# Performance work log

Hardware: AMD Instinct MI355X
Metric: run time of the kernel (lower is better)

The kernel has to match this reference:

```python
import jax, jax.numpy as jnp
import numpy as np

GRID_SIZE = 5
GRID_LO, GRID_HI = -1.0, 1.0


def setup_inputs() -> dict:
    key = jax.random.key(0)
    k1, k2 = jax.random.split(key)
    B, out_dim, in_dim, H, W = 8, 64, 64, 192, 192
    G = GRID_SIZE + 1
    x = jax.random.normal(k1, (B, in_dim, H, W), dtype=jnp.float32)
    coef = jax.random.normal(k2, (B, out_dim, in_dim, G), dtype=jnp.float32) * 0.1
    return {"x": x, "coef": coef}


def reference(x, coef):
    # x: [B, in_dim, H, W]; coef: [B, out_dim, in_dim, G] with G = grid_size + 1
    G = GRID_SIZE + 1
    grid = jnp.linspace(GRID_LO, GRID_HI, G, dtype=x.dtype)
    lo, hi = grid[0], grid[-1]
    spacing = grid[1] - grid[0]

    B, in_dim, H, W = x.shape
    out_dim = coef.shape[1]
    P = H * W

    xf = x.reshape(B, in_dim, P)
    xc = jnp.clip(xf, lo, hi)
    nx = (xc - lo) / spacing                      # normalized coordinate in [0, grid_size]
    idx = jnp.clip(jnp.floor(nx).astype(jnp.int32), 0, GRID_SIZE - 1)  # left knot
    frac = nx - idx.astype(x.dtype)               # fractional offset (grad flows via nx)
    w1 = 1.0 - frac
    w2 = frac
    idx_next = jnp.clip(idx + 1, 0, GRID_SIZE)    # right knot (max index = G-1)

    # Two-hot interpolation weights over the G grid points: [B, in, P, G]
    Wt = (w1[..., None] * jax.nn.one_hot(idx, G, dtype=x.dtype)
          + w2[..., None] * jax.nn.one_hot(idx_next, G, dtype=x.dtype))

    # result[b,o,p] = sum_i sum_g Wt[b,i,p,g] * coef[b,o,i,g]
    out = jnp.einsum('bipg,boig->bop', Wt, coef)
    return out.reshape(B, out_dim, H, W)
```

## Files before the change

kernel.cpp:

```cpp
#include <hip/hip_runtime.h>
#include <stdint.h>


typedef __fp16 half8_t __attribute__((ext_vector_type(8)));
typedef __fp16 half2_t __attribute__((ext_vector_type(2)));
typedef float f32x4 __attribute__((ext_vector_type(4)));

#define NBATCH 8
#define OD 64
#define ID 64
#define PIX 36864
#define NG 6
#define PT 192
#define KI 16
#define NCHUNK 4
#define AROW 104
#define XROW 18
#define PTILES (PIX / PT)

__global__ __launch_bounds__(256, 2)
void kan_mfma(const float* __restrict__ x, const float* __restrict__ coef,
              float* __restrict__ out) {
  const int t = threadIdx.x;
  const int lane = t & 63;
  const int wave = t >> 6;
  const int q8 = lane >> 4;
  const int col = lane & 15;

  const int bid = blockIdx.x;
  const int b = bid / PTILES;
  const int ptile = bid % PTILES;
  const int p0 = ptile * PT;

  __shared__ __fp16 A_lds[OD][AROW] __attribute__((aligned(16)));
  __shared__ float nx_lds[PT][XROW] __attribute__((aligned(16)));

  f32x4 acc[4][3];
#pragma unroll
  for (int i = 0; i < 4; ++i)
#pragma unroll
    for (int j = 0; j < 3; ++j)
      acc[i][j] = (f32x4){0.f, 0.f, 0.f, 0.f};

  const float* xb = x + (size_t)b * ID * PIX + p0;
  const float* cb = coef + (size_t)b * OD * ID * NG;

  const int iof0 = (q8 & 1) * 8;
  const int ghalf = q8 >> 1;

  for (int c = 0; c < NCHUNK; ++c) {
    const int i0 = c * KI;
    __syncthreads();

#pragma unroll
    for (int j = 0; j < (KI * PT) / 256; ++j) {
      int lin = j * 256 + t;
      int p = lin % PT;
      int iof = lin / PT;
      float xv = xb[(size_t)(i0 + iof) * PIX + p];
      xv = fminf(fmaxf(xv, -1.f), 1.f);
      nx_lds[p][iof] = (xv + 1.f) * 2.5f;
    }

    {
      const int o = t >> 2;
      const int r0 = (t & 3) * 24;
      const float* crow = cb + o * (ID * NG) + i0 * NG + r0;
#pragma unroll
      for (int j = 0; j < 24; ++j) {
        int r = r0 + j;
        int iof = r / 6;
        int g = r - iof * 6;
        A_lds[o][g * KI + iof] = (__fp16)crow[j];
      }
    }
    __syncthreads();

    float nxv[3][8];
#pragma unroll
    for (int pti = 0; pti < 3; ++pti) {
      int p = wave * 48 + pti * 16 + col;
#pragma unroll
      for (int j = 0; j < 8; ++j)
        nxv[pti][j] = nx_lds[p][iof0 + j];
    }

#pragma unroll
    for (int ks = 0; ks < 3; ++ks) {
      half8_t af[4];
#pragma unroll
      for (int ot = 0; ot < 4; ++ot)
        af[ot] = *(const half8_t*)&A_lds[ot * 16 + col][ks * 32 + q8 * 8];

      const float gf = (float)(2 * ks + ghalf);
#pragma unroll
      for (int pti = 0; pti < 3; ++pti) {
        union { half2_t h2[4]; half8_t v; } bu;
#pragma unroll
        for (int jj = 0; jj < 4; ++jj) {
          float h0 = fmaxf(0.f, 1.f - fabsf(nxv[pti][2 * jj] - gf));
          float h1 = fmaxf(0.f, 1.f - fabsf(nxv[pti][2 * jj + 1] - gf));
          bu.h2[jj] = __builtin_amdgcn_cvt_pkrtz(h0, h1);
        }
#pragma unroll
        for (int ot = 0; ot < 4; ++ot)
          acc[ot][pti] = __builtin_amdgcn_mfma_f32_16x16x32_f16(
              af[ot], bu.v, acc[ot][pti], 0, 0, 0);
      }
    }
  }

  float* ob = out + (size_t)b * OD * PIX + p0;
#pragma unroll
  for (int ot = 0; ot < 4; ++ot) {
#pragma unroll
    for (int pti = 0; pti < 3; ++pti) {
      int p = wave * 48 + pti * 16 + col;
#pragma unroll
      for (int r = 0; r < 4; ++r) {
        int o = ot * 16 + q8 * 4 + r;
        ob[(size_t)o * PIX + p] = acc[ot][pti][r];
      }
    }
  }
}

extern "C" void kernel_launch(void* const* d_in, const int* in_sizes, int n_in,
                              void* d_out, int out_size, void* d_ws, size_t ws_size,
                              hipStream_t stream) {
  const float* x = (const float*)d_in[0];
  const float* coef = (const float*)d_in[1];
  float* out = (float*)d_out;
  dim3 grid(NBATCH * PTILES);
  dim3 block(256);
  hipLaunchKernelGGL(kan_mfma, grid, block, 0, stream, x, coef, out);
}
```

Measured before the change: 154.0 us.

## Stage all coef once in LDS and load x directly into registers

The full per-batch coefficient block for all four input chunks is now loaded once into a wider LDS array with vectorized float4 loads and packed half2 stores, replacing the per-chunk scalar staging. The x tile is no longer staged through LDS: each lane reads its own pixels straight from global memory. This removes the per-chunk barriers. Occupancy hint is raised to 3 blocks per SM and output stores are made nontemporal. Direct x loads are strided per lane, so coalescing depends on the 16-lane col pattern, and the larger LDS footprint may limit occupancy.

```diff
diff --git a/kernel.cpp b/kernel.cpp
--- a/kernel.cpp
+++ b/kernel.cpp
@@ -14,11 +14,11 @@
 #define PT 192
 #define KI 16
 #define NCHUNK 4
-#define AROW 104
-#define XROW 18
+#define KC (KI * NG)
+#define AROW 392
 #define PTILES (PIX / PT)
 
-__global__ __launch_bounds__(256, 2)
+__global__ __launch_bounds__(256, 3)
 void kan_mfma(const float* __restrict__ x, const float* __restrict__ coef,
               float* __restrict__ out) {
   const int t = threadIdx.x;
@@ -33,7 +33,26 @@
   const int p0 = ptile * PT;
 
   __shared__ __fp16 A_lds[OD][AROW] __attribute__((aligned(16)));
-  __shared__ float nx_lds[PT][XROW] __attribute__((aligned(16)));
+
+  {
+    const int o = t >> 2;
+    const int c = t & 3;
+    const float* crow = coef + (size_t)b * (OD * ID * NG) + o * (ID * NG) + c * KC;
+    __fp16* arow = &A_lds[o][c * KC];
+#pragma unroll
+    for (int blk = 0; blk < 8; ++blk) {
+      f32x4 va = ((const f32x4*)crow)[blk * 3 + 0];
+      f32x4 vb = ((const f32x4*)crow)[blk * 3 + 1];
+      f32x4 vc = ((const f32x4*)crow)[blk * 3 + 2];
+      const float lo[NG] = {va[0], va[1], va[2], va[3], vb[0], vb[1]};
+      const float hi[NG] = {vb[2], vb[3], vc[0], vc[1], vc[2], vc[3]};
+#pragma unroll
+      for (int g = 0; g < NG; ++g) {
+        half2_t h2 = __builtin_amdgcn_cvt_pkrtz(lo[g], hi[g]);
+        *(half2_t*)&arow[g * KI + blk * 2] = h2;
+      }
+    }
+  }
 
   f32x4 acc[4][3];
 #pragma unroll
@@ -42,47 +61,26 @@
     for (int j = 0; j < 3; ++j)
       acc[i][j] = (f32x4){0.f, 0.f, 0.f, 0.f};
 
-  const float* xb = x + (size_t)b * ID * PIX + p0;
-  const float* cb = coef + (size_t)b * OD * ID * NG;
+  __syncthreads();
 
   const int iof0 = (q8 & 1) * 8;
   const int ghalf = q8 >> 1;
-
-  for (int c = 0; c < NCHUNK; ++c) {
-    const int i0 = c * KI;
-    __syncthreads();
+  const float* xb = x + (size_t)b * ID * PIX + p0 + wave * 48 + col
+                      + (size_t)iof0 * PIX;
 
 #pragma unroll
-    for (int j = 0; j < (KI * PT) / 256; ++j) {
-      int lin = j * 256 + t;
-      int p = lin % PT;
-      int iof = lin / PT;
-      float xv = xb[(size_t)(i0 + iof) * PIX + p];
-      xv = fminf(fmaxf(xv, -1.f), 1.f);
-      nx_lds[p][iof] = (xv + 1.f) * 2.5f;
-    }
-
-    {
-      const int o = t >> 2;
-      const int r0 = (t & 3) * 24;
-      const float* crow = cb + o * (ID * NG) + i0 * NG + r0;
-#pragma unroll
-      for (int j = 0; j < 24; ++j) {
-        int r = r0 + j;
-        int iof = r / 6;
-        int g = r - iof * 6;
-        A_lds[o][g * KI + iof] = (__fp16)crow[j];
-      }
-    }
-    __syncthreads();
-
+  for (int c = 0; c < NCHUNK; ++c) {
+    const float* xs = xb + (size_t)(c * KI) * PIX;
     float nxv[3][8];
 #pragma unroll
-    for (int pti = 0; pti < 3; ++pti) {
-      int p = wave * 48 + pti * 16 + col;
-#pragma unroll
-      for (int j = 0; j < 8; ++j)
-        nxv[pti][j] = nx_lds[p][iof0 + j];
+    for (int j = 0; j < 8; ++j) {
+      const float* xj = xs + (size_t)j * PIX;
+      float a0 = xj[0];
+      float a1 = xj[16];
+      float a2 = xj[32];
+      nxv[0][j] = (fminf(fmaxf(a0, -1.f), 1.f) + 1.f) * 2.5f;
+      nxv[1][j] = (fminf(fmaxf(a1, -1.f), 1.f) + 1.f) * 2.5f;
+      nxv[2][j] = (fminf(fmaxf(a2, -1.f), 1.f) + 1.f) * 2.5f;
     }
 
 #pragma unroll
@@ -90,7 +88,7 @@
       half8_t af[4];
 #pragma unroll
       for (int ot = 0; ot < 4; ++ot)
-        af[ot] = *(const half8_t*)&A_lds[ot * 16 + col][ks * 32 + q8 * 8];
+        af[ot] = *(const half8_t*)&A_lds[ot * 16 + col][c * KC + ks * 32 + q8 * 8];
 
       const float gf = (float)(2 * ks + ghalf);
 #pragma unroll
@@ -119,7 +117,7 @@
 #pragma unroll
       for (int r = 0; r < 4; ++r) {
         int o = ot * 16 + q8 * 4 + r;
-        ob[(size_t)o * PIX + p] = acc[ot][pti][r];
+        __builtin_nontemporal_store(acc[ot][pti][r], &ob[(size_t)o * PIX + p]);
       }
     }
   }
```

Result: slower. 161.2 us (+4.7%).
